# Performance work log

Measured on AMD Instinct MI355X. Metric: run time of the kernel, lower is better.

The kernel has to match this reference:

```python
import jax, jax.numpy as jnp
import numpy as np

B, C, D, H, W = 2, 3, 128, 192, 192
# spacing = (1, 1, 1) -> unit spacing, so jnp.gradient default is exact


def setup_inputs() -> dict:
    key = jax.random.key(0)
    # small displacements keep det(I + du) > 0 so log(det) is finite
    x = jax.random.normal(key, (B, C, D, H, W), dtype=jnp.float32) * 0.05
    return {"x": x}


def _jacobian_log_det_sq(x):
    # torch.gradient == numpy-style gradient: central differences in the
    # interior, one-sided differences at the boundaries.
    eye = jnp.eye(3, dtype=x.dtype)
    rows = []
    for j in range(3):  # derivative along spatial axis j (D, H, W)
        g = jnp.gradient(x, axis=2 + j)          # (B, C, D, H, W) = du_i/dx_j
        g = jnp.moveaxis(g, 1, -1)               # (B, D, H, W, i)
        rows.append(g + eye[j])                  # add delta_ij (identity)
    # J[..., j, i] = du_i/dx_j + delta_ij ; det is transpose-invariant
    J = jnp.stack(rows, axis=-2)                 # (B, D, H, W, 3, 3)
    det = jnp.linalg.det(J)                      # (B, D, H, W)
    return jnp.log(det) ** 2


def reference(x):
    return _jacobian_log_det_sq(x)
```

## Files before the change

kernel.cpp:

```cpp
#include <hip/hip_runtime.h>

constexpr int B = 2, C = 3, D = 128, H = 192, W = 192;
constexpr int sH = W;
constexpr int sD = H * W;
constexpr int sC = D * H * W;
constexpr int sB = C * sC;
constexpr int W4 = W / 4;
constexpr int NG = B * D * H * W4;

__global__ __launch_bounds__(256) void jac_logdet_sq(
    const float* __restrict__ x, float* __restrict__ out) {
    const int g = blockIdx.x * 256 + threadIdx.x;
    const int w4 = g % W4;
    int rid = g / W4;
    const int h = rid % H;
    rid /= H;
    const int d = rid % D;
    const int b = rid / D;
    const int w0 = w4 * 4;

    const int base = b * sB + d * sD + h * sH + w0;

    float gd[3][4], gh[3][4], gw[3][4];

    const int offL = (w0 > 0) ? -1 : 0;
    const int offR = (w0 + 4 < W) ? 4 : 3;
    const int offHp = (h < H - 1) ? sH : 0;
    const int offHm = (h > 0) ? sH : 0;
    const int offDp = (d < D - 1) ? sD : 0;
    const int offDm = (d > 0) ? sD : 0;
    const float ch = (h > 0 && h < H - 1) ? 0.5f : 1.0f;
    const float cd = (d > 0 && d < D - 1) ? 0.5f : 1.0f;

#pragma unroll
    for (int c = 0; c < 3; ++c) {
        const float* p = x + base + c * sC;
        const float4 vm  = *(const float4*)p;
        const float  lft = p[offL];
        const float  rgt = p[offR];
        const float4 vhp = *(const float4*)(p + offHp);
        const float4 vhm = *(const float4*)(p - offHm);
        const float4 vdp = *(const float4*)(p + offDp);
        const float4 vdm = *(const float4*)(p - offDm);

        gh[c][0] = (vhp.x - vhm.x) * ch;
        gh[c][1] = (vhp.y - vhm.y) * ch;
        gh[c][2] = (vhp.z - vhm.z) * ch;
        gh[c][3] = (vhp.w - vhm.w) * ch;

        gd[c][0] = (vdp.x - vdm.x) * cd;
        gd[c][1] = (vdp.y - vdm.y) * cd;
        gd[c][2] = (vdp.z - vdm.z) * cd;
        gd[c][3] = (vdp.w - vdm.w) * cd;

        gw[c][0] = (w0 == 0)     ? (vm.y - vm.x) : 0.5f * (vm.y - lft);
        gw[c][1] = 0.5f * (vm.z - vm.x);
        gw[c][2] = 0.5f * (vm.w - vm.y);
        gw[c][3] = (w0 + 4 == W) ? (vm.w - vm.z) : 0.5f * (rgt - vm.z);
    }

    float r[4];
#pragma unroll
    for (int e = 0; e < 4; ++e) {
        const float a00 = gd[0][e] + 1.0f, a01 = gd[1][e], a02 = gd[2][e];
        const float a10 = gh[0][e], a11 = gh[1][e] + 1.0f, a12 = gh[2][e];
        const float a20 = gw[0][e], a21 = gw[1][e], a22 = gw[2][e] + 1.0f;
        const float det = a00 * (a11 * a22 - a12 * a21)
                        - a01 * (a10 * a22 - a12 * a20)
                        + a02 * (a10 * a21 - a11 * a20);
        const float l = logf(det);
        r[e] = l * l;
    }

    *(float4*)(out + (long)g * 4) = make_float4(r[0], r[1], r[2], r[3]);
}

extern "C" void kernel_launch(void* const* d_in, const int* in_sizes, int n_in,
                              void* d_out, int out_size, void* d_ws, size_t ws_size,
                              hipStream_t stream) {
    const float* x = (const float*)d_in[0];
    float* out = (float*)d_out;
    jac_logdet_sq<<<dim3(NG / 256), dim3(256), 0, stream>>>(x, out);
}
```

Baseline: 180.7 us.

## March each thread along depth with register rolling window for D-neighbors

Each thread now processes a chunk of 8 consecutive depth slices for its 4-wide W segment. It keeps the previous, current and next D-planes in registers and shifts them each step, so each slice is loaded once instead of three times from global memory. This also cuts the thread count by 8x and switches logf to the faster __logf intrinsic. In exchange it has less parallelism, more registers per thread, and slightly lower log precision.

```diff
diff --git a/kernel.cpp b/kernel.cpp
--- a/kernel.cpp
+++ b/kernel.cpp
@@ -6,73 +6,110 @@
 constexpr int sC = D * H * W;
 constexpr int sB = C * sC;
 constexpr int W4 = W / 4;
-constexpr int NG = B * D * H * W4;
+constexpr int Dc = 8;
+constexpr int NCH = D / Dc;
+constexpr int NT = B * NCH * H * W4;
 
-__global__ __launch_bounds__(256) void jac_logdet_sq(
+__global__ __launch_bounds__(256, 4) void jac_logdet_sq(
     const float* __restrict__ x, float* __restrict__ out) {
     const int g = blockIdx.x * 256 + threadIdx.x;
     const int w4 = g % W4;
-    int rid = g / W4;
-    const int h = rid % H;
-    rid /= H;
-    const int d = rid % D;
-    const int b = rid / D;
     const int w0 = w4 * 4;
+    int t = g / W4;
+    const int h = t % H;
+    t /= H;
+    const int chunk = t % NCH;
+    const int b = t / NCH;
+    const int d0 = chunk * Dc;
 
-    const int base = b * sB + d * sD + h * sH + w0;
+    const int rowbase = b * sB + h * sH + w0;
 
-    float gd[3][4], gh[3][4], gw[3][4];
-
-    const int offL = (w0 > 0) ? -1 : 0;
-    const int offR = (w0 + 4 < W) ? 4 : 3;
+    const int offL  = (w0 > 0) ? -1 : 0;
+    const int offR  = (w0 + 4 < W) ? 4 : 3;
     const int offHp = (h < H - 1) ? sH : 0;
     const int offHm = (h > 0) ? sH : 0;
-    const int offDp = (d < D - 1) ? sD : 0;
-    const int offDm = (d > 0) ? sD : 0;
-    const float ch = (h > 0 && h < H - 1) ? 0.5f : 1.0f;
-    const float cd = (d > 0 && d < D - 1) ? 0.5f : 1.0f;
+    const float chc = (h > 0 && h < H - 1) ? 0.5f : 1.0f;
+
+    float cm[3][4], c0[3][4];
+#pragma unroll
+    for (int c = 0; c < 3; ++c) {
+        const float* p = x + rowbase + c * sC + d0 * sD;
+        const float4 v0 = *(const float4*)p;
+        c0[c][0] = v0.x; c0[c][1] = v0.y; c0[c][2] = v0.z; c0[c][3] = v0.w;
+        if (d0 > 0) {
+            const float4 vm = *(const float4*)(p - sD);
+            cm[c][0] = vm.x; cm[c][1] = vm.y; cm[c][2] = vm.z; cm[c][3] = vm.w;
+        } else {
+            cm[c][0] = v0.x; cm[c][1] = v0.y; cm[c][2] = v0.z; cm[c][3] = v0.w;
+        }
+    }
+
+    int obase = ((b * D + d0) * H + h) * W + w0;
+
+    for (int dd = 0; dd < Dc; ++dd) {
+        const int d = d0 + dd;
+        const float cdc = (d > 0 && d < D - 1) ? 0.5f : 1.0f;
+
+        float cp[3][4], hp[3][4], hm[3][4], lft[3], rgt[3];
+#pragma unroll
+        for (int c = 0; c < 3; ++c) {
+            const float* p = x + rowbase + c * sC + d * sD;
+            if (d < D - 1) {
+                const float4 v = *(const float4*)(p + sD);
+                cp[c][0] = v.x; cp[c][1] = v.y; cp[c][2] = v.z; cp[c][3] = v.w;
+            } else {
+                cp[c][0] = c0[c][0]; cp[c][1] = c0[c][1];
+                cp[c][2] = c0[c][2]; cp[c][3] = c0[c][3];
+            }
+            const float4 vhp = *(const float4*)(p + offHp);
+            const float4 vhm = *(const float4*)(p - offHm);
+            hp[c][0] = vhp.x; hp[c][1] = vhp.y; hp[c][2] = vhp.z; hp[c][3] = vhp.w;
+            hm[c][0] = vhm.x; hm[c][1] = vhm.y; hm[c][2] = vhm.z; hm[c][3] = vhm.w;
+            lft[c] = p[offL];
+            rgt[c] = p[offR];
+        }
+
+        float r[4];
+#pragma unroll
+        for (int e = 0; e < 4; ++e) {
+            float gd[3], gh[3], gw[3];
+#pragma unroll
+            for (int c = 0; c < 3; ++c) {
+                gd[c] = (cp[c][e] - cm[c][e]) * cdc;
+                gh[c] = (hp[c][e] - hm[c][e]) * chc;
+            }
+#pragma unroll
+            for (int c = 0; c < 3; ++c) {
+                if (e == 0)
+                    gw[c] = (w0 == 0) ? (c0[c][1] - c0[c][0])
+                                      : 0.5f * (c0[c][1] - lft[c]);
+                else if (e == 1) gw[c] = 0.5f * (c0[c][2] - c0[c][0]);
+                else if (e == 2) gw[c] = 0.5f * (c0[c][3] - c0[c][1]);
+                else
+                    gw[c] = (w0 + 4 == W) ? (c0[c][3] - c0[c][2])
+                                          : 0.5f * (rgt[c] - c0[c][2]);
+            }
+            const float a00 = gd[0] + 1.0f, a01 = gd[1], a02 = gd[2];
+            const float a10 = gh[0], a11 = gh[1] + 1.0f, a12 = gh[2];
+            const float a20 = gw[0], a21 = gw[1], a22 = gw[2] + 1.0f;
+            const float det = a00 * (a11 * a22 - a12 * a21)
+                            - a01 * (a10 * a22 - a12 * a20)
+                            + a02 * (a10 * a21 - a11 * a20);
+            const float l = __logf(det);
+            r[e] = l * l;
+        }
+
+        *(float4*)(out + obase + dd * sD) = make_float4(r[0], r[1], r[2], r[3]);
 
 #pragma unroll
-    for (int c = 0; c < 3; ++c) {
-        const float* p = x + base + c * sC;
-        const float4 vm  = *(const float4*)p;
-        const float  lft = p[offL];
-        const float  rgt = p[offR];
-        const float4 vhp = *(const float4*)(p + offHp);
-        const float4 vhm = *(const float4*)(p - offHm);
-        const float4 vdp = *(const float4*)(p + offDp);
-        const float4 vdm = *(const float4*)(p - offDm);
-
-        gh[c][0] = (vhp.x - vhm.x) * ch;
-        gh[c][1] = (vhp.y - vhm.y) * ch;
-        gh[c][2] = (vhp.z - vhm.z) * ch;
-        gh[c][3] = (vhp.w - vhm.w) * ch;
-
-        gd[c][0] = (vdp.x - vdm.x) * cd;
-        gd[c][1] = (vdp.y - vdm.y) * cd;
-        gd[c][2] = (vdp.z - vdm.z) * cd;
-        gd[c][3] = (vdp.w - vdm.w) * cd;
-
-        gw[c][0] = (w0 == 0)     ? (vm.y - vm.x) : 0.5f * (vm.y - lft);
-        gw[c][1] = 0.5f * (vm.z - vm.x);
-        gw[c][2] = 0.5f * (vm.w - vm.y);
-        gw[c][3] = (w0 + 4 == W) ? (vm.w - vm.z) : 0.5f * (rgt - vm.z);
+        for (int c = 0; c < 3; ++c) {
+#pragma unroll
+            for (int e = 0; e < 4; ++e) {
+                cm[c][e] = c0[c][e];
+                c0[c][e] = cp[c][e];
+            }
+        }
     }
-
-    float r[4];
-#pragma unroll
-    for (int e = 0; e < 4; ++e) {
-        const float a00 = gd[0][e] + 1.0f, a01 = gd[1][e], a02 = gd[2][e];
-        const float a10 = gh[0][e], a11 = gh[1][e] + 1.0f, a12 = gh[2][e];
-        const float a20 = gw[0][e], a21 = gw[1][e], a22 = gw[2][e] + 1.0f;
-        const float det = a00 * (a11 * a22 - a12 * a21)
-                        - a01 * (a10 * a22 - a12 * a20)
-                        + a02 * (a10 * a21 - a11 * a20);
-        const float l = logf(det);
-        r[e] = l * l;
-    }
-
-    *(float4*)(out + (long)g * 4) = make_float4(r[0], r[1], r[2], r[3]);
 }
 
 extern "C" void kernel_launch(void* const* d_in, const int* in_sizes, int n_in,
@@ -80,5 +117,5 @@
                               hipStream_t stream) {
     const float* x = (const float*)d_in[0];
     float* out = (float*)d_out;
-    jac_logdet_sq<<<dim3(NG / 256), dim3(256), 0, stream>>>(x, out);
+    jac_logdet_sq<<<dim3(NT / 256), dim3(256), 0, stream>>>(x, out);
 }
```

New measurement: 186.6 us. 1.03x slower.

## Tile stencil with LDS halo, march along depth with register sliding window

Applied to the files above, without the earlier changes.

Replaces the one-thread-per-4-voxels kernel with 16x16-tile blocks that march 4 depth slices. The d-neighbours are kept in a register sliding window, and the h/w neighbours come from a double-buffered LDS tile with a halo. The goal is to cut the redundant global loads of the 7-point stencil. The change also swaps logf for __logf, which costs some accuracy. It adds a __syncthreads per slice and only 4 slices of reuse, so the halo rows reloaded per chunk still add overhead.

```diff
diff --git a/kernel.cpp b/kernel.cpp
--- a/kernel.cpp
+++ b/kernel.cpp
@@ -5,74 +5,148 @@
 constexpr int sD = H * W;
 constexpr int sC = D * H * W;
 constexpr int sB = C * sC;
-constexpr int W4 = W / 4;
-constexpr int NG = B * D * H * W4;
 
-__global__ __launch_bounds__(256) void jac_logdet_sq(
+constexpr int TH = 16;
+constexpr int TW = 16;
+constexpr int DC = 4;
+constexpr int HX = H / TH;
+constexpr int WX = (W / 4) / TW;
+constexpr int NDC = D / DC;
+constexpr int NB = B * NDC * HX * WX;
+constexpr int ROWS = TH + 2;
+constexpr int RSTR = TW + 1;
+constexpr int CH_STR = ROWS * RSTR;
+constexpr int BUFSZ = C * CH_STR;
+
+__global__ __launch_bounds__(256, 4) void jac_logdet_sq(
     const float* __restrict__ x, float* __restrict__ out) {
-    const int g = blockIdx.x * 256 + threadIdx.x;
-    const int w4 = g % W4;
-    int rid = g / W4;
-    const int h = rid % H;
-    rid /= H;
-    const int d = rid % D;
-    const int b = rid / D;
-    const int w0 = w4 * 4;
+    __shared__ float4 lds[2][BUFSZ];
 
-    const int base = b * sB + d * sD + h * sH + w0;
+    const int tid = threadIdx.x;
+    const int tx = tid & 15;
+    const int ty = tid >> 4;
 
-    float gd[3][4], gh[3][4], gw[3][4];
+    int bb = blockIdx.x;
+    const int wx = bb % WX; bb /= WX;
+    const int hx = bb % HX; bb /= HX;
+    const int dch = bb % NDC;
+    const int b = bb / NDC;
 
-    const int offL = (w0 > 0) ? -1 : 0;
-    const int offR = (w0 + 4 < W) ? 4 : 3;
-    const int offHp = (h < H - 1) ? sH : 0;
-    const int offHm = (h > 0) ? sH : 0;
-    const int offDp = (d < D - 1) ? sD : 0;
-    const int offDm = (d > 0) ? sD : 0;
-    const float ch = (h > 0 && h < H - 1) ? 0.5f : 1.0f;
-    const float cd = (d > 0 && d < D - 1) ? 0.5f : 1.0f;
+    const int d0 = dch * DC;
+    const int h0 = hx * TH;
+    const int h = h0 + ty;
+    const int w0 = (wx * TW + tx) * 4;
+
+    const float* pb = x + b * sB;
+    const int cidx = h * sH + w0;
+
+    const int hc = tid / 32;
+    const int hr = (tid >> 4) & 1;
+    const int htx = tid & 15;
+    const int hh = hr ? ((h0 + TH < H) ? h0 + TH : H - 1)
+                      : ((h0 > 0) ? h0 - 1 : 0);
+    const int hidx = hh * sH + (wx * TW + htx) * 4;
+    const int hlds = hc * CH_STR + (hr ? (TH + 1) : 0) * RSTR + htx;
+
+    const float chc = (h > 0 && h < H - 1) ? 0.5f : 1.0f;
+
+    float4 cm[3], c0[3], cp[3];
+
+    const int dm = (d0 > 0) ? d0 - 1 : 0;
+#pragma unroll
+    for (int c = 0; c < 3; ++c) {
+        c0[c] = *(const float4*)(pb + c * sC + d0 * sD + cidx);
+        cm[c] = *(const float4*)(pb + c * sC + dm * sD + cidx);
+    }
+#pragma unroll
+    for (int c = 0; c < 3; ++c)
+        lds[0][c * CH_STR + (ty + 1) * RSTR + tx] = c0[c];
+    if (tid < 96)
+        lds[0][hlds] = *(const float4*)(pb + hc * sC + d0 * sD + hidx);
+    __syncthreads();
+
+    int cur = 0;
+    int obase = ((b * D + d0) * H + h) * W + w0;
+
+    for (int dd = 0; dd < DC; ++dd) {
+        const int d = d0 + dd;
+        const int dp = (d + 1 < D) ? d + 1 : D - 1;
+        const float cdc = (d > 0 && d < D - 1) ? 0.5f : 1.0f;
 
 #pragma unroll
-    for (int c = 0; c < 3; ++c) {
-        const float* p = x + base + c * sC;
-        const float4 vm  = *(const float4*)p;
-        const float  lft = p[offL];
-        const float  rgt = p[offR];
-        const float4 vhp = *(const float4*)(p + offHp);
-        const float4 vhm = *(const float4*)(p - offHm);
-        const float4 vdp = *(const float4*)(p + offDp);
-        const float4 vdm = *(const float4*)(p - offDm);
+        for (int c = 0; c < 3; ++c)
+            cp[c] = *(const float4*)(pb + c * sC + dp * sD + cidx);
+        float4 hv;
+        const bool do_stage = (dd < DC - 1);
+        if (do_stage && tid < 96)
+            hv = *(const float4*)(pb + hc * sC + dp * sD + hidx);
 
-        gh[c][0] = (vhp.x - vhm.x) * ch;
-        gh[c][1] = (vhp.y - vhm.y) * ch;
-        gh[c][2] = (vhp.z - vhm.z) * ch;
-        gh[c][3] = (vhp.w - vhm.w) * ch;
+        float lg[3], rg[3];
+        if (tx == 0 && w0 > 0) {
+#pragma unroll
+            for (int c = 0; c < 3; ++c) lg[c] = pb[c * sC + d * sD + cidx - 1];
+        }
+        if (tx == 15 && w0 + 4 < W) {
+#pragma unroll
+            for (int c = 0; c < 3; ++c) rg[c] = pb[c * sC + d * sD + cidx + 4];
+        }
 
-        gd[c][0] = (vdp.x - vdm.x) * cd;
-        gd[c][1] = (vdp.y - vdm.y) * cd;
-        gd[c][2] = (vdp.z - vdm.z) * cd;
-        gd[c][3] = (vdp.w - vdm.w) * cd;
+        const float4* bufc = lds[cur];
+        float gd[3][4], gh[3][4], gw[3][4];
+#pragma unroll
+        for (int c = 0; c < 3; ++c) {
+            const float4 hp = bufc[c * CH_STR + (ty + 2) * RSTR + tx];
+            const float4 hm = bufc[c * CH_STR + (ty    ) * RSTR + tx];
+            gh[c][0] = (hp.x - hm.x) * chc;
+            gh[c][1] = (hp.y - hm.y) * chc;
+            gh[c][2] = (hp.z - hm.z) * chc;
+            gh[c][3] = (hp.w - hm.w) * chc;
 
-        gw[c][0] = (w0 == 0)     ? (vm.y - vm.x) : 0.5f * (vm.y - lft);
-        gw[c][1] = 0.5f * (vm.z - vm.x);
-        gw[c][2] = 0.5f * (vm.w - vm.y);
-        gw[c][3] = (w0 + 4 == W) ? (vm.w - vm.z) : 0.5f * (rgt - vm.z);
+            gd[c][0] = (cp[c].x - cm[c].x) * cdc;
+            gd[c][1] = (cp[c].y - cm[c].y) * cdc;
+            gd[c][2] = (cp[c].z - cm[c].z) * cdc;
+            gd[c][3] = (cp[c].w - cm[c].w) * cdc;
+
+            const float lft = (tx == 0) ? lg[c]
+                : bufc[c * CH_STR + (ty + 1) * RSTR + tx - 1].w;
+            const float rgt = (tx == 15) ? rg[c]
+                : bufc[c * CH_STR + (ty + 1) * RSTR + tx + 1].x;
+            gw[c][0] = (w0 == 0)     ? (c0[c].y - c0[c].x)
+                                     : 0.5f * (c0[c].y - lft);
+            gw[c][1] = 0.5f * (c0[c].z - c0[c].x);
+            gw[c][2] = 0.5f * (c0[c].w - c0[c].y);
+            gw[c][3] = (w0 + 4 == W) ? (c0[c].w - c0[c].z)
+                                     : 0.5f * (rgt - c0[c].z);
+        }
+
+        float r[4];
+#pragma unroll
+        for (int e = 0; e < 4; ++e) {
+            const float a00 = gd[0][e] + 1.0f, a01 = gd[1][e], a02 = gd[2][e];
+            const float a10 = gh[0][e], a11 = gh[1][e] + 1.0f, a12 = gh[2][e];
+            const float a20 = gw[0][e], a21 = gw[1][e], a22 = gw[2][e] + 1.0f;
+            const float det = a00 * (a11 * a22 - a12 * a21)
+                            - a01 * (a10 * a22 - a12 * a20)
+                            + a02 * (a10 * a21 - a11 * a20);
+            const float l = __logf(det);
+            r[e] = l * l;
+        }
+        *(float4*)(out + obase) = make_float4(r[0], r[1], r[2], r[3]);
+        obase += sD;
+
+        if (do_stage) {
+            const int nxt = cur ^ 1;
+#pragma unroll
+            for (int c = 0; c < 3; ++c)
+                lds[nxt][c * CH_STR + (ty + 1) * RSTR + tx] = cp[c];
+            if (tid < 96) lds[nxt][hlds] = hv;
+            __syncthreads();
+            cur = nxt;
+        }
+
+#pragma unroll
+        for (int c = 0; c < 3; ++c) { cm[c] = c0[c]; c0[c] = cp[c]; }
     }
-
-    float r[4];
-#pragma unroll
-    for (int e = 0; e < 4; ++e) {
-        const float a00 = gd[0][e] + 1.0f, a01 = gd[1][e], a02 = gd[2][e];
-        const float a10 = gh[0][e], a11 = gh[1][e] + 1.0f, a12 = gh[2][e];
-        const float a20 = gw[0][e], a21 = gw[1][e], a22 = gw[2][e] + 1.0f;
-        const float det = a00 * (a11 * a22 - a12 * a21)
-                        - a01 * (a10 * a22 - a12 * a20)
-                        + a02 * (a10 * a21 - a11 * a20);
-        const float l = logf(det);
-        r[e] = l * l;
-    }
-
-    *(float4*)(out + (long)g * 4) = make_float4(r[0], r[1], r[2], r[3]);
 }
 
 extern "C" void kernel_launch(void* const* d_in, const int* in_sizes, int n_in,
@@ -80,5 +154,5 @@
                               hipStream_t stream) {
     const float* x = (const float*)d_in[0];
     float* out = (float*)d_out;
-    jac_logdet_sq<<<dim3(NG / 256), dim3(256), 0, stream>>>(x, out);
+    jac_logdet_sq<<<dim3(NB), dim3(256), 0, stream>>>(x, out);
 }
```

Result: no change. 179.6 us (-0.6%).
